# Kernel optimization log

Hardware: AMD Instinct MI355X
Metric: run time of the kernel (lower is better)

The kernel has to match this reference:

```python
import jax, jax.numpy as jnp
import numpy as np

RADIUS = 0.2
NSAMPLE = 64


def _ball_query(xyz, new_xyz):
    """PointNet++-style ball query: first NSAMPLE point indices within RADIUS
    of each center; empty slots filled with the first found index.
    xyz: (B, N, 3), new_xyz: (B, P, 3) -> idx: (B, P, NSAMPLE) int32."""
    N = xyz.shape[1]
    # squared distances (B, P, N)
    d2 = jnp.sum((new_xyz[:, :, None, :] - xyz[:, None, :, :]) ** 2, axis=-1)
    # score = point index if inside ball else sentinel N; smallest NSAMPLE scores
    # give the first NSAMPLE in-ball indices in ascending order (CUDA order).
    scores = jnp.where(d2 < RADIUS * RADIUS, jnp.arange(N, dtype=jnp.int32), N)
    neg_vals, _ = jax.lax.top_k(-scores, NSAMPLE)
    idx = -neg_vals  # ascending smallest scores
    first = idx[..., :1]
    return jnp.where(idx < N, idx, first)


def setup_inputs() -> dict:
    key = jax.random.key(0)
    k1, k2, k3 = jax.random.split(key, 3)
    B, N, P, C = 4, 16384, 1024, 128
    xyz = jax.random.uniform(k1, (B, N, 3), dtype=jnp.float32)
    new_xyz = jax.random.uniform(k2, (B, P, 3), dtype=jnp.float32)
    features = jax.random.normal(k3, (B, C, N), dtype=jnp.float32)
    return {"xyz": xyz, "new_xyz": new_xyz, "features": features}


def reference(xyz, new_xyz, features):
    B, N, _ = xyz.shape
    idx0 = _ball_query(xyz, new_xyz)  # (B, P, S), returned as bq_idx
    # dedup: slots (other than slot 0) equal to the first index are the
    # padding fills -> redirect them to the shadow point at index N
    first = idx0[..., :1]
    dup = (idx0 == first).at[..., 0].set(False)
    idx = jnp.where(dup, N, idx0)

    # shadow xyz = 1e6, shadow feature = 0
    xyz_pad = jnp.concatenate([xyz, jnp.full((B, 1, 3), 1.0e6, xyz.dtype)], axis=1)
    grouped_xyz = jax.vmap(lambda p, i: p[i])(xyz_pad, idx)        # (B, P, S, 3)
    grouped_xyz = grouped_xyz.transpose(0, 3, 1, 2)                # (B, 3, P, S)
    grouped_xyz = grouped_xyz - new_xyz.transpose(0, 2, 1)[..., None]

    feats_pad = jnp.concatenate([features, jnp.zeros_like(features[:, :, :1])], axis=-1)
    grouped_feat = jax.vmap(lambda p, i: p[i])(feats_pad.transpose(0, 2, 1), idx)  # (B, P, S, C)
    grouped_feat = grouped_feat.transpose(0, 3, 1, 2)              # (B, C, P, S)

    # use_xyz=True: zero shadow coords, normalize by radius, concat
    xyz_feature = jnp.where(grouped_xyz > 1.0e5, 0.0, grouped_xyz) / RADIUS
    new_features = jnp.concatenate([xyz_feature, grouped_feat], axis=1)  # (B, 3+C, P, S)
    return new_features, grouped_xyz, idx0
```

## Files before the change

kernel.cpp:

```cpp
#include <hip/hip_runtime.h>
#include <cstdint>

#define BQ_B 4
#define BQ_N 16384
#define BQ_P 1024
#define BQ_C 128
#define NS   64
#define R2   0.04f

#define O1 ((size_t)BQ_B * 131 * BQ_P * NS)
#define O2 (O1 + (size_t)BQ_B * 3 * BQ_P * NS)


__global__ __launch_bounds__(256) void ballquery_kernel(
    const float* __restrict__ xyz,
    const float* __restrict__ new_xyz,
    int* __restrict__ wsIdx,
    float* __restrict__ out)
{
#pragma clang fp contract(off)
    const int lane = threadIdx.x & 63;
    const int w    = threadIdx.x >> 6;
    const int center = blockIdx.x * 4 + w;
    const int b = center >> 10;
    const int p = center & (BQ_P - 1);

    __shared__ int lidx[4][NS];

    const float cx = new_xyz[center * 3 + 0];
    const float cy = new_xyz[center * 3 + 1];
    const float cz = new_xyz[center * 3 + 2];
    const float* xb = xyz + (size_t)b * BQ_N * 3;

    const unsigned long long lmask = (1ull << lane) - 1ull;
    int total = 0;

    for (int base = 0; base < BQ_N; base += 512) {
        float d2a[8];
        #pragma unroll
        for (int u = 0; u < 8; ++u) {
            const int i = base + u * 64 + lane;
            const float dx = xb[i * 3 + 0] - cx;
            const float dy = xb[i * 3 + 1] - cy;
            const float dz = xb[i * 3 + 2] - cz;
            d2a[u] = dx * dx + dy * dy + dz * dz;
        }
        #pragma unroll
        for (int u = 0; u < 8; ++u) {
            const unsigned long long m = __ballot(d2a[u] < R2);
            if ((m >> lane) & 1ull) {
                const int r = total + (int)__popcll(m & lmask);
                if (r < NS) lidx[w][r] = base + u * 64 + lane;
            }
            total += (int)__popcll(m);
        }
        if (total >= NS) break;
    }
    __threadfence_block();

    const int tt    = (total > NS) ? NS : total;
    const int first = (total > 0) ? lidx[w][0] : BQ_N;
    const int v     = (lane < tt) ? lidx[w][lane] : BQ_N;
    const int idx0  = (lane < tt) ? v : first;
    const bool real = v < BQ_N;

    wsIdx[(size_t)center * NS + lane] = v;
    out[O2 + (size_t)center * NS + lane] = (float)idx0;

    #pragma unroll
    for (int d = 0; d < 3; ++d) {
        const float c  = (d == 0) ? cx : ((d == 1) ? cy : cz);
        const float pt = real ? xb[v * 3 + d] : 1000000.0f;
        const float g  = pt - c;
        out[O1 + ((size_t)(b * 3 + d) * BQ_P + p) * NS + lane] = g;
        const float xf = ((g > 100000.0f) ? 0.0f : g) / 0.2f;
        out[((size_t)(b * 131 + d) * BQ_P + p) * NS + lane] = xf;
    }
}

__global__ __launch_bounds__(512) void feat_gather_kernel(
    const float* __restrict__ features,
    const int* __restrict__ wsIdx,
    float* __restrict__ out)
{
    const int b = blockIdx.x >> 7;
    const int c = blockIdx.x & 127;
    const int t = threadIdx.x;

    __shared__ float row[BQ_N];

    const float4* fr = (const float4*)(features + ((size_t)b * BQ_C + c) * BQ_N);
    float4* row4 = (float4*)row;
    #pragma unroll
    for (int k = 0; k < 8; ++k)
        row4[k * 512 + t] = fr[k * 512 + t];
    __syncthreads();

    const int4* gi4 = (const int4*)(wsIdx + (size_t)b * BQ_P * NS);
    float4* op = (float4*)(out + (size_t)(b * 131 + 3 + c) * BQ_P * NS);
    #pragma unroll 4
    for (int k = 0; k < 32; ++k) {
        const int q = k * 512 + t;
        const int4 gi = gi4[q];
        float4 v;
        v.x = (gi.x < BQ_N) ? row[gi.x] : 0.0f;
        v.y = (gi.y < BQ_N) ? row[gi.y] : 0.0f;
        v.z = (gi.z < BQ_N) ? row[gi.z] : 0.0f;
        v.w = (gi.w < BQ_N) ? row[gi.w] : 0.0f;
        op[q] = v;
    }
}

extern "C" void kernel_launch(void* const* d_in, const int* in_sizes, int n_in,
                              void* d_out, int out_size, void* d_ws, size_t ws_size,
                              hipStream_t stream) {
    const float* xyz      = (const float*)d_in[0];
    const float* new_xyz  = (const float*)d_in[1];
    const float* features = (const float*)d_in[2];
    float* out = (float*)d_out;
    int*   wsIdx = (int*)d_ws;

    ballquery_kernel<<<dim3(BQ_B * BQ_P / 4), dim3(256), 0, stream>>>(xyz, new_xyz, wsIdx, out);
    feat_gather_kernel<<<dim3(BQ_B * BQ_C), dim3(512), 0, stream>>>(features, wsIdx, out);
}
```

Baseline: 196.2 us.

## Software-pipeline point and index loads, use nontemporal stores for outputs

The ball-query loop now prefetches the next 512 points' coordinates into registers while the current chunk is tested, and the feature-gather kernel double-buffers its index loads and issues them before the feature row copy. All large output writes and the feature row read use nontemporal load/store builtins to avoid polluting caches. This aims to hide global memory latency in both kernels, at the cost of more registers and possibly lower occupancy.

```diff
diff --git a/kernel.cpp b/kernel.cpp
--- a/kernel.cpp
+++ b/kernel.cpp
@@ -10,6 +10,9 @@
 
 #define O1 ((size_t)BQ_B * 131 * BQ_P * NS)
 #define O2 (O1 + (size_t)BQ_B * 3 * BQ_P * NS)
+
+typedef float v4f __attribute__((ext_vector_type(4)));
+typedef int   v4i __attribute__((ext_vector_type(4)));
 
 
 __global__ __launch_bounds__(256) void ballquery_kernel(
@@ -35,26 +38,48 @@
     const unsigned long long lmask = (1ull << lane) - 1ull;
     int total = 0;
 
-    for (int base = 0; base < BQ_N; base += 512) {
-        float d2a[8];
+    float px[8], py[8], pz[8];
+    #pragma unroll
+    for (int u = 0; u < 8; ++u) {
+        const int i = u * 64 + lane;
+        px[u] = xb[i * 3 + 0];
+        py[u] = xb[i * 3 + 1];
+        pz[u] = xb[i * 3 + 2];
+    }
+
+    int base = 0;
+    for (;;) {
+        const int nbase = base + 512;
+        float nx[8], ny[8], nz[8];
+        if (nbase < BQ_N) {
+            #pragma unroll
+            for (int u = 0; u < 8; ++u) {
+                const int i = nbase + u * 64 + lane;
+                nx[u] = xb[i * 3 + 0];
+                ny[u] = xb[i * 3 + 1];
+                nz[u] = xb[i * 3 + 2];
+            }
+        }
+        unsigned long long m[8];
         #pragma unroll
         for (int u = 0; u < 8; ++u) {
-            const int i = base + u * 64 + lane;
-            const float dx = xb[i * 3 + 0] - cx;
-            const float dy = xb[i * 3 + 1] - cy;
-            const float dz = xb[i * 3 + 2] - cz;
-            d2a[u] = dx * dx + dy * dy + dz * dz;
+            const float dx = px[u] - cx;
+            const float dy = py[u] - cy;
+            const float dz = pz[u] - cz;
+            m[u] = __ballot(dx * dx + dy * dy + dz * dz < R2);
         }
         #pragma unroll
         for (int u = 0; u < 8; ++u) {
-            const unsigned long long m = __ballot(d2a[u] < R2);
-            if ((m >> lane) & 1ull) {
-                const int r = total + (int)__popcll(m & lmask);
+            if ((m[u] >> lane) & 1ull) {
+                const int r = total + (int)__popcll(m[u] & lmask);
                 if (r < NS) lidx[w][r] = base + u * 64 + lane;
             }
-            total += (int)__popcll(m);
+            total += (int)__popcll(m[u]);
         }
-        if (total >= NS) break;
+        if (total >= NS || nbase >= BQ_N) break;
+        base = nbase;
+        #pragma unroll
+        for (int u = 0; u < 8; ++u) { px[u] = nx[u]; py[u] = ny[u]; pz[u] = nz[u]; }
     }
     __threadfence_block();
 
@@ -65,16 +90,18 @@
     const bool real = v < BQ_N;
 
     wsIdx[(size_t)center * NS + lane] = v;
-    out[O2 + (size_t)center * NS + lane] = (float)idx0;
+    __builtin_nontemporal_store((float)idx0, &out[O2 + (size_t)center * NS + lane]);
 
     #pragma unroll
     for (int d = 0; d < 3; ++d) {
         const float c  = (d == 0) ? cx : ((d == 1) ? cy : cz);
         const float pt = real ? xb[v * 3 + d] : 1000000.0f;
         const float g  = pt - c;
-        out[O1 + ((size_t)(b * 3 + d) * BQ_P + p) * NS + lane] = g;
+        __builtin_nontemporal_store(g,
+            &out[O1 + ((size_t)(b * 3 + d) * BQ_P + p) * NS + lane]);
         const float xf = ((g > 100000.0f) ? 0.0f : g) / 0.2f;
-        out[((size_t)(b * 131 + d) * BQ_P + p) * NS + lane] = xf;
+        __builtin_nontemporal_store(xf,
+            &out[((size_t)(b * 131 + d) * BQ_P + p) * NS + lane]);
     }
 }
 
@@ -89,25 +116,40 @@
 
     __shared__ float row[BQ_N];
 
-    const float4* fr = (const float4*)(features + ((size_t)b * BQ_C + c) * BQ_N);
-    float4* row4 = (float4*)row;
+    const v4i* gi4 = (const v4i*)(wsIdx + (size_t)b * BQ_P * NS);
+    v4i g[4];
+    #pragma unroll
+    for (int j = 0; j < 4; ++j) g[j] = gi4[j * 512 + t];
+
+    const v4f* fr = (const v4f*)(features + ((size_t)b * BQ_C + c) * BQ_N);
+    v4f* row4 = (v4f*)row;
     #pragma unroll
     for (int k = 0; k < 8; ++k)
-        row4[k * 512 + t] = fr[k * 512 + t];
+        row4[k * 512 + t] = __builtin_nontemporal_load(&fr[k * 512 + t]);
     __syncthreads();
 
-    const int4* gi4 = (const int4*)(wsIdx + (size_t)b * BQ_P * NS);
-    float4* op = (float4*)(out + (size_t)(b * 131 + 3 + c) * BQ_P * NS);
-    #pragma unroll 4
-    for (int k = 0; k < 32; ++k) {
-        const int q = k * 512 + t;
-        const int4 gi = gi4[q];
-        float4 v;
-        v.x = (gi.x < BQ_N) ? row[gi.x] : 0.0f;
-        v.y = (gi.y < BQ_N) ? row[gi.y] : 0.0f;
-        v.z = (gi.z < BQ_N) ? row[gi.z] : 0.0f;
-        v.w = (gi.w < BQ_N) ? row[gi.w] : 0.0f;
-        op[q] = v;
+    v4f* op = (v4f*)(out + (size_t)(b * 131 + 3 + c) * BQ_P * NS);
+    for (int kk = 0; kk < 32; kk += 4) {
+        v4i n[4];
+        const bool more = (kk + 4) < 32;
+        if (more) {
+            #pragma unroll
+            for (int j = 0; j < 4; ++j) n[j] = gi4[(kk + 4 + j) * 512 + t];
+        }
+        #pragma unroll
+        for (int j = 0; j < 4; ++j) {
+            const v4i gi = g[j];
+            v4f v;
+            v.x = (gi.x < BQ_N) ? row[gi.x] : 0.0f;
+            v.y = (gi.y < BQ_N) ? row[gi.y] : 0.0f;
+            v.z = (gi.z < BQ_N) ? row[gi.z] : 0.0f;
+            v.w = (gi.w < BQ_N) ? row[gi.w] : 0.0f;
+            __builtin_nontemporal_store(v, &op[(kk + j) * 512 + t]);
+        }
+        if (more) {
+            #pragma unroll
+            for (int j = 0; j < 4; ++j) g[j] = n[j];
+        }
     }
 }
 
```

After: 197.7 us. About the same (+0.7%).
